# Kernel tuning notes

Measured on AMD Instinct MI355X. Metric: run time of the kernel, lower is better.

Reference implementation:

```python
import jax, jax.numpy as jnp
import numpy as np

N_NODES = 100000
N_EDGES = 1600000
D_FEAT = 64


def setup_inputs() -> dict:
    key = jax.random.key(0)
    k1, k2, k3, k4, k5 = jax.random.split(key, 5)
    feat = jax.random.normal(k1, (N_NODES, D_FEAT), dtype=jnp.float32)
    weight = jax.random.normal(k2, (N_EDGES, 1), dtype=jnp.float32)
    bias = jax.random.normal(k3, (D_FEAT,), dtype=jnp.float32)
    src = jax.random.randint(k4, (N_EDGES,), 0, N_NODES, dtype=jnp.int32)
    dst = jax.random.randint(k5, (N_EDGES,), 0, N_NODES, dtype=jnp.int32)
    return {"feat": feat, "weight": weight, "bias": bias, "src": src, "dst": dst}


def reference(feat, weight, bias, src, dst):
    # Weighted SpMM: out[v] = sum_{e: dst[e]==v} weight[e] * feat[src[e]] + bias
    messages = feat[src] * weight  # [E, D] gather + per-edge scale
    out = jax.ops.segment_sum(messages, dst, num_segments=N_NODES)  # [N, D]
    return out + bias
```

## Files before the change

kernel.cpp:

```cpp
#include <hip/hip_runtime.h>

#define N_NODES 100000
#define N_EDGES 1600000
#define D_FEAT  64
#define NFEAT_ELEM (N_NODES * D_FEAT)

#define BUCK_SHIFT 6
#define BUCK_NODES 64
#define NBUCK ((N_NODES + BUCK_NODES - 1) / BUCK_NODES)
#define NB1 (NBUCK + 1)

#define CHUNK   8192
#define NCHUNK  ((N_EDGES + CHUNK - 1) / CHUNK)
#define BIN_BLK 512
#define BIN_EPT (CHUNK / BIN_BLK)
#define SCAN_PER ((NBUCK + BIN_BLK - 1) / BIN_BLK)
#define PREP_BLOCKS 128

#define GB_BLK   512
#define GB_NODES 128
#define NGRP ((NBUCK + 1) / 2)
#define GB_CAP   2816
#define GB_EPT   6

#define TT_CT ((NCHUNK + 63) / 64)
#define TT_BT ((NB1 + 63) / 64)

typedef float          vf4 __attribute__((ext_vector_type(4)));
typedef float          vf2 __attribute__((ext_vector_type(2)));
typedef int            vi2 __attribute__((ext_vector_type(2)));
typedef unsigned short vu4 __attribute__((ext_vector_type(4)));
typedef unsigned short ushort_t;

#define TBL_BYTES  (NCHUNK * NB1 * 2)
#define OFF_TBL    0
#define OFF_TBLT   (((OFF_TBL + TBL_BYTES) + 255) & ~255)
#define OFF_EP     (((OFF_TBLT + NB1 * NCHUNK * 2) + 255) & ~255)
#define OFF_FEATB  (OFF_EP + N_EDGES * 8)
#define WS_MED     (size_t)OFF_FEATB
#define WS_FULL    (size_t)(OFF_FEATB + (size_t)NFEAT_ELEM * 2)

template <int BF16>
__global__ __launch_bounds__(BIN_BLK) void k_bin(const int* __restrict__ src,
                                                 const int* __restrict__ dst,
                                                 const float* __restrict__ weight,
                                                 const float* __restrict__ feat,
                                                 ushort_t* __restrict__ featb,
                                                 ushort_t* __restrict__ tbl,
                                                 vi2* __restrict__ ep) {
    if (blockIdx.x >= NCHUNK) {
        if (!BF16) return;
        const int stride = PREP_BLOCKS * BIN_BLK;
        for (int i = (blockIdx.x - NCHUNK) * BIN_BLK + threadIdx.x;
             i < NFEAT_ELEM / 4; i += stride) {
            vf4 x = ((const vf4*)feat)[i];
            vu4 r;
#pragma unroll
            for (int k = 0; k < 4; ++k) {
                unsigned bb = __float_as_uint(x[k]);
                r[k] = (ushort_t)((bb + 0x7fffu + ((bb >> 16) & 1u)) >> 16);
            }
            ((vu4*)featb)[i] = r;
        }
        return;
    }

    __shared__ vi2 schunk[CHUNK];
    __shared__ int lcnt[NBUCK];
    __shared__ int ss[BIN_BLK];
    const int t = threadIdx.x;
    const int c = blockIdx.x;
    const int e0 = c * CHUNK;
    const int chunkN = (N_EDGES - e0 < CHUNK) ? (N_EDGES - e0) : CHUNK;

    for (int i = t; i < NBUCK; i += BIN_BLK) lcnt[i] = 0;
    __syncthreads();

    int bk[BIN_EPT], rk[BIN_EPT], xk[BIN_EPT], wk[BIN_EPT];
#pragma unroll
    for (int k = 0; k < BIN_EPT; ++k) {
        const int e = e0 + t + k * BIN_BLK;
        bk[k] = -1;
        if (e < N_EDGES) {
            int v = __builtin_nontemporal_load(dst + e);
            int s = __builtin_nontemporal_load(src + e);
            wk[k] = __builtin_nontemporal_load((const int*)weight + e);
            bk[k] = v >> BUCK_SHIFT;
            xk[k] = ((v & (BUCK_NODES - 1)) << 24) | s;
            rk[k] = atomicAdd(&lcnt[bk[k]], 1);
        }
    }
    __syncthreads();

    int v7[SCAN_PER];
    const int lo = t * SCAN_PER;
    int s = 0;
#pragma unroll
    for (int k = 0; k < SCAN_PER; ++k) {
        const int i = lo + k;
        v7[k] = (i < NBUCK) ? lcnt[i] : 0;
        s += v7[k];
    }
    ss[t] = s;
    __syncthreads();
    for (int off = 1; off < BIN_BLK; off <<= 1) {
        int x = (t >= off) ? ss[t - off] : 0;
        __syncthreads();
        ss[t] += x;
        __syncthreads();
    }
    int run = ss[t] - s;
    ushort_t* row = tbl + (size_t)c * NB1;
#pragma unroll
    for (int k = 0; k < SCAN_PER; ++k) {
        const int i = lo + k;
        if (i < NBUCK) {
            row[i] = (ushort_t)run;
            lcnt[i] = run;
            run += v7[k];
        }
    }
    if (t == BIN_BLK - 1) row[NBUCK] = (ushort_t)chunkN;
    __syncthreads();

#pragma unroll
    for (int k = 0; k < BIN_EPT; ++k)
        if (bk[k] >= 0) schunk[lcnt[bk[k]] + rk[k]] = (vi2){xk[k], wk[k]};
    __syncthreads();

    for (int i = t; i < chunkN; i += BIN_BLK)
        ep[e0 + i] = schunk[i];
}

__global__ __launch_bounds__(256) void k_ttrans(const ushort_t* __restrict__ tbl,
                                                ushort_t* __restrict__ tblT) {
    __shared__ ushort_t tile[64][65];
    const int t = threadIdx.x;
    const int c0 = (blockIdx.x % TT_CT) * 64;
    const int b0 = (blockIdx.x / TT_CT) * 64;
    for (int idx = t; idx < 4096; idx += 256) {
        int cl = idx >> 6, bl = idx & 63;
        int c = c0 + cl, bb = b0 + bl;
        tile[bl][cl] = (c < NCHUNK && bb < NB1) ? tbl[(size_t)c * NB1 + bb] : (ushort_t)0;
    }
    __syncthreads();
    for (int idx = t; idx < 4096; idx += 256) {
        int bl = idx >> 6, cl = idx & 63;
        int c = c0 + cl, bb = b0 + bl;
        if (c < NCHUNK && bb < NB1) tblT[(size_t)bb * NCHUNK + c] = tile[bl][cl];
    }
}

template <int BF16>
__global__ __launch_bounds__(GB_BLK, 8) void k_sgather(const float* __restrict__ feat,
                                                       const ushort_t* __restrict__ featb,
                                                       const float* __restrict__ bias,
                                                       const ushort_t* __restrict__ tblT,
                                                       const vi2* __restrict__ ep,
                                                       float* __restrict__ out) {
    __shared__ vi2      srt[GB_CAP];
    __shared__ int      basearr[GB_BLK];
    __shared__ ushort_t o0arr[GB_BLK];
    __shared__ ushort_t o1arr[GB_BLK];
    __shared__ int      cnt[GB_NODES], off[GB_NODES];

    const int t = threadIdx.x;
    const int lane = t & 63;
    const int wid = t >> 6;
    const int grp = blockIdx.x;
    const int b0 = grp * 2;
    const int bhi = (b0 + 2 <= NBUCK) ? b0 + 2 : NBUCK;
    if (t < GB_NODES) cnt[t] = 0;

    int o0 = 0, o1 = 0, o2 = 0;
    if (t < NCHUNK) {
        o0 = tblT[(size_t)b0 * NCHUNK + t];
        o1 = tblT[(size_t)(b0 + 1) * NCHUNK + t];
        o2 = tblT[(size_t)bhi * NCHUNK + t];
    }
    o0arr[t] = (ushort_t)o0;
    o1arr[t] = (ushort_t)o1;
    const int len = o2 - o0;
    basearr[t] = len;
    __syncthreads();
    for (int o = 1; o < GB_BLK; o <<= 1) {
        int x = (t >= o) ? basearr[t - o] : 0;
        __syncthreads();
        basearr[t] += x;
        __syncthreads();
    }
    const int nTot = basearr[GB_BLK - 1];
    const int myexc = basearr[t] - len;
    __syncthreads();
    basearr[t] = myexc;
    __syncthreads();

    const int nStg = nTot < GB_CAP ? nTot : GB_CAP;
    int   xk[GB_EPT];
    float wk[GB_EPT];
    int   rk[GB_EPT];
#pragma unroll
    for (int k = 0; k < GB_EPT; ++k) {
        const int p = t + k * GB_BLK;
        xk[k] = -1;
        if (p < nStg) {
            int c = 0;
#pragma unroll
            for (int s2 = 256; s2 > 0; s2 >>= 1) {
                int m = c + s2;
                if (m < GB_BLK && basearr[m] <= p) c = m;
            }
            const int e = (int)o0arr[c] + (p - basearr[c]);
            vi2 v = ep[(size_t)c * CHUNK + e];
            int r = ((e >= (int)o1arr[c]) ? 64 : 0) + (int)((unsigned)v.x >> 24);
            xk[k] = (v.x & 0xFFFFFF) | (r << 24);
            wk[k] = __int_as_float(v.y);
            rk[k] = atomicAdd(&cnt[r], 1);
        }
    }
    __syncthreads();

    if (t < GB_NODES) off[t] = cnt[t];
    __syncthreads();
    for (int d = 1; d < GB_NODES; d <<= 1) {
        int x = 0;
        if (t < GB_NODES && t >= d) x = off[t - d];
        __syncthreads();
        if (t < GB_NODES) off[t] += x;
        __syncthreads();
    }

#pragma unroll
    for (int k = 0; k < GB_EPT; ++k) {
        if (xk[k] != -1) {
            int r = (unsigned)xk[k] >> 24;
            srt[off[r] - cnt[r] + rk[k]] = (vi2){xk[k], __float_as_int(wk[k])};
        }
    }
    __syncthreads();

    const int col = lane & 31;
    const int half = lane >> 5;
    const vf2 b2 = ((const vf2*)bias)[col];
    for (int rp = 0; rp < 8; ++rp) {
        const int rA = wid * 16 + rp;
        const int rB = rA + 8;
        const int ccA = cnt[rA], s0A = off[rA] - ccA;
        const int ccB = cnt[rB], s0B = off[rB] - ccB;
        float a0A = 0.f, a1A = 0.f, a0B = 0.f, a1B = 0.f;
        const int ccM = ccA > ccB ? ccA : ccB;
        for (int i = 0; i < ccM; i += 8) {
            float wA[4], wB[4];
            unsigned dA[4], dB[4];
            vf2 fA[4], fB[4];
#pragma unroll
            for (int k = 0; k < 4; ++k) {
                const int ei = i + 2 * k + half;
                vi2 e = (ei < ccA) ? srt[s0A + ei] : (vi2){0, 0};
                wA[k] = __int_as_float(e.y);
                const int sidx = e.x & 0xFFFFFF;
                if (BF16) dA[k] = *((const unsigned*)(featb + (size_t)sidx * D_FEAT) + col);
                else      fA[k] = *((const vf2*)(feat + (size_t)sidx * D_FEAT) + col);
            }
#pragma unroll
            for (int k = 0; k < 4; ++k) {
                const int ei = i + 2 * k + half;
                vi2 e = (ei < ccB) ? srt[s0B + ei] : (vi2){0, 0};
                wB[k] = __int_as_float(e.y);
                const int sidx = e.x & 0xFFFFFF;
                if (BF16) dB[k] = *((const unsigned*)(featb + (size_t)sidx * D_FEAT) + col);
                else      fB[k] = *((const vf2*)(feat + (size_t)sidx * D_FEAT) + col);
            }
            if (BF16) {
#pragma unroll
                for (int k = 0; k < 4; ++k) {
                    a0A = fmaf(wA[k], __uint_as_float(dA[k] << 16), a0A);
                    a1A = fmaf(wA[k], __uint_as_float(dA[k] & 0xFFFF0000u), a1A);
                    a0B = fmaf(wB[k], __uint_as_float(dB[k] << 16), a0B);
                    a1B = fmaf(wB[k], __uint_as_float(dB[k] & 0xFFFF0000u), a1B);
                }
            } else {
#pragma unroll
                for (int k = 0; k < 4; ++k) {
                    a0A = fmaf(wA[k], fA[k].x, a0A);
                    a1A = fmaf(wA[k], fA[k].y, a1A);
                    a0B = fmaf(wB[k], fB[k].x, a0B);
                    a1B = fmaf(wB[k], fB[k].y, a1B);
                }
            }
        }
        a0A += __shfl_xor(a0A, 32);
        a1A += __shfl_xor(a1A, 32);
        a0B += __shfl_xor(a0B, 32);
        a1B += __shfl_xor(a1B, 32);
        const int nodeA = grp * GB_NODES + rA;
        const int nodeB = grp * GB_NODES + rB;
        if (half == 0 && nodeA < N_NODES) {
            vf2 o = {a0A + b2.x, a1A + b2.y};
            __builtin_nontemporal_store(o, (vf2*)(out + (size_t)nodeA * D_FEAT) + col);
        }
        if (half == 0 && nodeB < N_NODES) {
            vf2 o = {a0B + b2.x, a1B + b2.y};
            __builtin_nontemporal_store(o, (vf2*)(out + (size_t)nodeB * D_FEAT) + col);
        }
    }
    __syncthreads();

    for (int p = GB_CAP + t; p < nTot; p += GB_BLK) {
        int c = 0;
#pragma unroll
        for (int s2 = 256; s2 > 0; s2 >>= 1) {
            int m = c + s2;
            if (m < GB_BLK && basearr[m] <= p) c = m;
        }
        const int e = (int)o0arr[c] + (p - basearr[c]);
        vi2 v = ep[(size_t)c * CHUNK + e];
        int r = ((e >= (int)o1arr[c]) ? 64 : 0) + (int)((unsigned)v.x >> 24);
        int node = grp * GB_NODES + r;
        float w = __int_as_float(v.y);
        int sidx = v.x & 0xFFFFFF;
        if (node < N_NODES)
            for (int d2 = 0; d2 < D_FEAT; ++d2)
                atomicAdd(&out[(size_t)node * D_FEAT + d2], w * feat[(size_t)sidx * D_FEAT + d2]);
    }
}

__global__ void init_out_kernel(const float* __restrict__ bias,
                                float* __restrict__ out) {
    int i = blockIdx.x * blockDim.x + threadIdx.x;
    if (i < N_NODES * D_FEAT) out[i] = bias[i & (D_FEAT - 1)];
}

__global__ void edge_scatter_kernel(const float* __restrict__ feat,
                                    const float* __restrict__ weight,
                                    const int* __restrict__ src,
                                    const int* __restrict__ dst,
                                    float* __restrict__ out) {
    int e = blockIdx.x * 4 + (threadIdx.x >> 6);
    int lane = threadIdx.x & 63;
    if (e < N_EDGES) {
        atomicAdd(&out[dst[e] * D_FEAT + lane], weight[e] * feat[src[e] * D_FEAT + lane]);
    }
}

extern "C" void kernel_launch(void* const* d_in, const int* in_sizes, int n_in,
                              void* d_out, int out_size, void* d_ws, size_t ws_size,
                              hipStream_t stream) {
    const float* feat   = (const float*)d_in[0];
    const float* weight = (const float*)d_in[1];
    const float* bias   = (const float*)d_in[2];
    const int*   src    = (const int*)d_in[3];
    const int*   dst    = (const int*)d_in[4];
    float* out = (float*)d_out;

    if (ws_size < WS_MED) {
        int total = N_NODES * D_FEAT;
        init_out_kernel<<<(total + 255) / 256, 256, 0, stream>>>(bias, out);
        edge_scatter_kernel<<<(N_EDGES + 3) / 4, 256, 0, stream>>>(feat, weight, src, dst, out);
        return;
    }

    char* ws = (char*)d_ws;
    ushort_t* tbl   = (ushort_t*)(ws + OFF_TBL);
    ushort_t* tblT  = (ushort_t*)(ws + OFF_TBLT);
    vi2*      ep    = (vi2*)(ws + OFF_EP);
    ushort_t* featb = (ushort_t*)(ws + OFF_FEATB);
    const bool use_bf16 = (ws_size >= WS_FULL);

    if (use_bf16) {
        k_bin<1><<<NCHUNK + PREP_BLOCKS, BIN_BLK, 0, stream>>>(src, dst, weight, feat, featb, tbl, ep);
        k_ttrans<<<TT_CT * TT_BT, 256, 0, stream>>>(tbl, tblT);
        k_sgather<1><<<NGRP, GB_BLK, 0, stream>>>(feat, featb, bias, tblT, ep, out);
    } else {
        k_bin<0><<<NCHUNK, BIN_BLK, 0, stream>>>(src, dst, weight, feat, featb, tbl, ep);
        k_ttrans<<<TT_CT * TT_BT, 256, 0, stream>>>(tbl, tblT);
        k_sgather<0><<<NGRP, GB_BLK, 0, stream>>>(feat, featb, bias, tblT, ep, out);
    }
}
```

Baseline: 71.52 us.

## Drop bucket-table transpose kernel and use wave-shuffle scans in gather

The separate transpose of the chunk×bucket offset table is removed. The gather kernel now reads each chunk's row directly from the original table, loading two adjacent 16-bit offsets as one 32-bit word. This removes a kernel launch and a full table write and read, but each block now makes strided, uncoalesced reads, which are expected to be served from L2. The two shared-memory Hillis-Steele scans, each needing many barriers, are replaced by wavefront shuffle scans combined through a small per-wave sum array.

After: 64.08 us. 10.4% less time.

```diff
diff --git a/kernel.cpp b/kernel.cpp
--- a/kernel.cpp
+++ b/kernel.cpp
@@ -23,9 +23,6 @@
 #define GB_CAP   2816
 #define GB_EPT   6
 
-#define TT_CT ((NCHUNK + 63) / 64)
-#define TT_BT ((NB1 + 63) / 64)
-
 typedef float          vf4 __attribute__((ext_vector_type(4)));
 typedef float          vf2 __attribute__((ext_vector_type(2)));
 typedef int            vi2 __attribute__((ext_vector_type(2)));
@@ -34,8 +31,7 @@
 
 #define TBL_BYTES  (NCHUNK * NB1 * 2)
 #define OFF_TBL    0
-#define OFF_TBLT   (((OFF_TBL + TBL_BYTES) + 255) & ~255)
-#define OFF_EP     (((OFF_TBLT + NB1 * NCHUNK * 2) + 255) & ~255)
+#define OFF_EP     (((OFF_TBL + TBL_BYTES) + 255) & ~255)
 #define OFF_FEATB  (OFF_EP + N_EDGES * 8)
 #define WS_MED     (size_t)OFF_FEATB
 #define WS_FULL    (size_t)(OFF_FEATB + (size_t)NFEAT_ELEM * 2)
@@ -132,30 +128,11 @@
         ep[e0 + i] = schunk[i];
 }
 
-__global__ __launch_bounds__(256) void k_ttrans(const ushort_t* __restrict__ tbl,
-                                                ushort_t* __restrict__ tblT) {
-    __shared__ ushort_t tile[64][65];
-    const int t = threadIdx.x;
-    const int c0 = (blockIdx.x % TT_CT) * 64;
-    const int b0 = (blockIdx.x / TT_CT) * 64;
-    for (int idx = t; idx < 4096; idx += 256) {
-        int cl = idx >> 6, bl = idx & 63;
-        int c = c0 + cl, bb = b0 + bl;
-        tile[bl][cl] = (c < NCHUNK && bb < NB1) ? tbl[(size_t)c * NB1 + bb] : (ushort_t)0;
-    }
-    __syncthreads();
-    for (int idx = t; idx < 4096; idx += 256) {
-        int bl = idx >> 6, cl = idx & 63;
-        int c = c0 + cl, bb = b0 + bl;
-        if (c < NCHUNK && bb < NB1) tblT[(size_t)bb * NCHUNK + c] = tile[bl][cl];
-    }
-}
-
 template <int BF16>
 __global__ __launch_bounds__(GB_BLK, 8) void k_sgather(const float* __restrict__ feat,
                                                        const ushort_t* __restrict__ featb,
                                                        const float* __restrict__ bias,
-                                                       const ushort_t* __restrict__ tblT,
+                                                       const ushort_t* __restrict__ tbl,
                                                        const vi2* __restrict__ ep,
                                                        float* __restrict__ out) {
     __shared__ vi2      srt[GB_CAP];
@@ -163,36 +140,46 @@
     __shared__ ushort_t o0arr[GB_BLK];
     __shared__ ushort_t o1arr[GB_BLK];
     __shared__ int      cnt[GB_NODES], off[GB_NODES];
+    __shared__ int      wsum[8];
+    __shared__ int      wpre[9];
+    __shared__ int      c64tot;
 
     const int t = threadIdx.x;
     const int lane = t & 63;
     const int wid = t >> 6;
     const int grp = blockIdx.x;
     const int b0 = grp * 2;
-    const int bhi = (b0 + 2 <= NBUCK) ? b0 + 2 : NBUCK;
     if (t < GB_NODES) cnt[t] = 0;
 
     int o0 = 0, o1 = 0, o2 = 0;
     if (t < NCHUNK) {
-        o0 = tblT[(size_t)b0 * NCHUNK + t];
-        o1 = tblT[(size_t)(b0 + 1) * NCHUNK + t];
-        o2 = tblT[(size_t)bhi * NCHUNK + t];
+        const ushort_t* rowp = tbl + (size_t)t * NB1 + b0;
+        unsigned u = *(const unsigned*)rowp;
+        o0 = (int)(u & 0xFFFFu);
+        o1 = (int)(u >> 16);
+        o2 = (b0 + 2 <= NBUCK) ? (int)rowp[2] : o1;
     }
     o0arr[t] = (ushort_t)o0;
     o1arr[t] = (ushort_t)o1;
     const int len = o2 - o0;
-    basearr[t] = len;
-    __syncthreads();
-    for (int o = 1; o < GB_BLK; o <<= 1) {
-        int x = (t >= o) ? basearr[t - o] : 0;
-        __syncthreads();
-        basearr[t] += x;
-        __syncthreads();
-    }
-    const int nTot = basearr[GB_BLK - 1];
-    const int myexc = basearr[t] - len;
-    __syncthreads();
-    basearr[t] = myexc;
+
+    int incl = len;
+#pragma unroll
+    for (int o = 1; o < 64; o <<= 1) {
+        int x = __shfl_up(incl, o);
+        if (lane >= o) incl += x;
+    }
+    if (lane == 63) wsum[wid] = incl;
+    __syncthreads();
+    if (t == 0) {
+        int run = 0;
+#pragma unroll
+        for (int i2 = 0; i2 < 8; ++i2) { wpre[i2] = run; run += wsum[i2]; }
+        wpre[8] = run;
+    }
+    __syncthreads();
+    const int nTot = wpre[8];
+    basearr[t] = wpre[wid] + incl - len;
     __syncthreads();
 
     const int nStg = nTot < GB_CAP ? nTot : GB_CAP;
@@ -220,13 +207,18 @@
     }
     __syncthreads();
 
-    if (t < GB_NODES) off[t] = cnt[t];
-    __syncthreads();
-    for (int d = 1; d < GB_NODES; d <<= 1) {
-        int x = 0;
-        if (t < GB_NODES && t >= d) x = off[t - d];
+    {
+        int v = (t < GB_NODES) ? cnt[t] : 0;
+        int inc2 = v;
+#pragma unroll
+        for (int o = 1; o < 64; o <<= 1) {
+            int x = __shfl_up(inc2, o);
+            if (lane >= o) inc2 += x;
+        }
+        if (t == 63) c64tot = inc2;
         __syncthreads();
-        if (t < GB_NODES) off[t] += x;
+        if (t >= 64 && t < 128) inc2 += c64tot;
+        if (t < GB_NODES) off[t] = inc2;
         __syncthreads();
     }
 
@@ -362,18 +354,15 @@
 
     char* ws = (char*)d_ws;
     ushort_t* tbl   = (ushort_t*)(ws + OFF_TBL);
-    ushort_t* tblT  = (ushort_t*)(ws + OFF_TBLT);
     vi2*      ep    = (vi2*)(ws + OFF_EP);
     ushort_t* featb = (ushort_t*)(ws + OFF_FEATB);
     const bool use_bf16 = (ws_size >= WS_FULL);
 
     if (use_bf16) {
         k_bin<1><<<NCHUNK + PREP_BLOCKS, BIN_BLK, 0, stream>>>(src, dst, weight, feat, featb, tbl, ep);
-        k_ttrans<<<TT_CT * TT_BT, 256, 0, stream>>>(tbl, tblT);
-        k_sgather<1><<<NGRP, GB_BLK, 0, stream>>>(feat, featb, bias, tblT, ep, out);
+        k_sgather<1><<<NGRP, GB_BLK, 0, stream>>>(feat, featb, bias, tbl, ep, out);
     } else {
         k_bin<0><<<NCHUNK, BIN_BLK, 0, stream>>>(src, dst, weight, feat, featb, tbl, ep);
-        k_ttrans<<<TT_CT * TT_BT, 256, 0, stream>>>(tbl, tblT);
-        k_sgather<0><<<NGRP, GB_BLK, 0, stream>>>(feat, featb, bias, tblT, ep, out);
-    }
-}
+        k_sgather<0><<<NGRP, GB_BLK, 0, stream>>>(feat, featb, bias, tbl, ep, out);
+    }
+}
```
